# Performance work log

Measured on AMD Instinct MI355X. Metric: run time of the kernel, lower is better.

## Reference

```python
import jax, jax.numpy as jnp
import numpy as np

H, O, E, V = 128, 128, 512, 34
B, T, L = 64, 2048, 256


def _lstm(x, wih, whh, bih, bhh):
    # x: [T, B, Din] -> outputs [T, B, H]; PyTorch gate order i, f, g, o
    n = whh.shape[1]
    h0 = jnp.zeros((x.shape[1], n), x.dtype)
    b = bih + bhh
    def step(carry, xt):
        h, c = carry
        g = xt @ wih.T + h @ whh.T + b
        i, f, gg, o = jnp.split(g, 4, axis=-1)
        c = jax.nn.sigmoid(f) * c + jax.nn.sigmoid(i) * jnp.tanh(gg)
        h = jax.nn.sigmoid(o) * jnp.tanh(c)
        return (h, c), h
    _, ys = jax.lax.scan(step, (h0, h0), x)
    return ys


def _conv1d_s2(x, w, b):
    # x: [B, Cin, T], w: [Cout, Cin, 2], kernel=2 stride=2 valid
    y = jax.lax.conv_general_dilated(x, w, (2,), 'VALID', dimension_numbers=('NCH', 'OIH', 'NCH'))
    return y + b[None, :, None]


def setup_inputs():
    key = jax.random.key(0)
    ctr = [0]
    def mk(shape, s=0.05):
        ctr[0] += 1
        return jax.random.normal(jax.random.fold_in(key, ctr[0]), shape, dtype=jnp.float32) * s
    inp = {}
    inp['utter'] = mk((B, T, 40), 1.0)
    inp['targets'] = jax.random.randint(jax.random.fold_in(key, 999), (B, L), 0, V)
    inp['wih_f'] = mk((4 * H, 40)); inp['whh_f'] = mk((4 * H, H)); inp['bih_f'] = mk((4 * H,)); inp['bhh_f'] = mk((4 * H,))
    inp['wih_r'] = mk((4 * H, 40)); inp['whh_r'] = mk((4 * H, H)); inp['bih_r'] = mk((4 * H,)); inp['bhh_r'] = mk((4 * H,))
    inp['c1w'] = mk((H, 2 * H, 2)); inp['c1b'] = mk((H,))
    inp['wih1'] = mk((4 * H, H)); inp['whh1'] = mk((4 * H, H)); inp['bih1'] = mk((4 * H,)); inp['bhh1'] = mk((4 * H,))
    inp['c2w'] = mk((H, H, 2)); inp['c2b'] = mk((H,))
    inp['wih2'] = mk((4 * H, H)); inp['whh2'] = mk((4 * H, H)); inp['bih2'] = mk((4 * H,)); inp['bhh2'] = mk((4 * H,))
    inp['kw'] = mk((O, H)); inp['kb'] = mk((O,)); inp['vw'] = mk((O, H)); inp['vb'] = mk((O,))
    inp['wihd'] = mk((4 * O, O + E)); inp['whhd'] = mk((4 * O, O)); inp['bihd'] = mk((4 * O,)); inp['bhhd'] = mk((4 * O,))
    inp['w1'] = mk((V, O)); inp['b1'] = mk((V,)); inp['w2'] = mk((V, O)); inp['b2'] = mk((V,))
    inp['w3'] = mk((V, V)); inp['b3'] = mk((V,))
    inp['emb'] = mk((V, E), 1.0)
    inp['sh0'] = mk((B, O)); inp['sc0'] = mk((B, O))
    return inp


def _forward(utter, targets, wih_f, whh_f, bih_f, bhh_f, wih_r, whh_r, bih_r, bhh_r,
             c1w, c1b, wih1, whh1, bih1, bhh1, c2w, c2b, wih2, whh2, bih2, bhh2,
             kw, kb, vw, vb, wihd, whhd, bihd, bhhd, w1, b1, w2, b2, w3, b3,
             emb, sh0, sc0):
    # ---- Listener (encoder) ----
    x = jnp.transpose(utter, (1, 0, 2))            # [T, B, 40]
    fwd = _lstm(x, wih_f, whh_f, bih_f, bhh_f)
    bwd = _lstm(x[::-1], wih_r, whh_r, bih_r, bhh_r)[::-1]
    h = jnp.concatenate([fwd, bwd], axis=-1)       # [T, B, 2H]
    h = jnp.transpose(h, (1, 2, 0))                # [B, 2H, T]
    h = _conv1d_s2(h, c1w, c1b)                    # [B, H, T/2]
    h = jnp.transpose(h, (2, 0, 1))                # [T/2, B, H]
    h = _lstm(h, wih1, whh1, bih1, bhh1)
    h = jnp.transpose(h, (1, 2, 0))
    h = _conv1d_s2(h, c2w, c2b)                    # [B, H, T/4]
    h = jnp.transpose(h, (2, 0, 1))
    h = _lstm(h, wih2, whh2, bih2, bhh2)
    h = jnp.transpose(h, (1, 0, 2))                # [B, T/4, H]
    hk = h @ kw.T + kb                              # [B, T/4, O]
    hv = h @ vw.T + vb
    # ---- Speller (decoder) ----
    ys = jnp.transpose(emb[targets], (1, 0, 2))[:-1]   # [L-1, B, E]
    mask = jnp.ones((utter.shape[0], hk.shape[1]), utter.dtype)  # all full-length
    bd = bihd + bhhd
    def step(carry, y_in):
        c, sh, sc = carry
        g = jnp.concatenate([y_in, c], axis=1) @ wihd.T + sh @ whhd.T + bd
        i, f, gg, o = jnp.split(g, 4, axis=-1)
        sc_n = jax.nn.sigmoid(f) * sc + jax.nn.sigmoid(i) * jnp.tanh(gg)
        sh_n = jax.nn.sigmoid(o) * jnp.tanh(sc_n)
        # NOTE: original attends with the cell state sc (faithful to source)
        att = jax.nn.softmax(jnp.einsum('btd,bd->bt', hk, sc_n), axis=1) * mask
        att = att / jnp.sum(att, axis=1, keepdims=True)
        c_n = jnp.einsum('bt,btd->bd', att, hv)
        out = jax.nn.relu(sh_n @ w1.T + b1 + c_n @ w2.T + b2)
        out = jax.nn.softmax(out @ w3.T + b3, axis=1)
        return (c_n, sh_n, sc_n), out
    c0 = jnp.zeros_like(sh0)
    _, preds = jax.lax.scan(step, (c0, sh0, sc0), ys)
    return jnp.transpose(preds, (1, 0, 2))         # [B, L-1, V]


def reference(utter, targets, wih_f, whh_f, bih_f, bhh_f, wih_r, whh_r, bih_r, bhh_r,
              c1w, c1b, wih1, whh1, bih1, bhh1, c2w, c2b, wih2, whh2, bih2, bhh2,
              kw, kb, vw, vb, wihd, whhd, bihd, bhhd, w1, b1, w2, b2, w3, b3,
              emb, sh0, sc0):
    return _forward(utter, targets, wih_f, whh_f, bih_f, bhh_f, wih_r, whh_r, bih_r, bhh_r,
                    c1w, c1b, wih1, whh1, bih1, bhh1, c2w, c2b, wih2, whh2, bih2, bhh2,
                    kw, kb, vw, vb, wihd, whhd, bihd, bhhd, w1, b1, w2, b2, w3, b3,
                    emb, sh0, sc0)
```

## Files before the change

kernel.cpp:

```cpp
#include <hip/hip_runtime.h>

typedef _Float16 half_t;
typedef _Float16 __attribute__((ext_vector_type(2))) half2_t;

__device__ __forceinline__ float fdot2_(half2_t a, half2_t b, float c) {
#if __has_builtin(__builtin_amdgcn_fdot2)
    return __builtin_amdgcn_fdot2(a, b, c, false);
#else
    return c + (float)a[0] * (float)b[0] + (float)a[1] * (float)b[1];
#endif
}
__device__ __forceinline__ half2_t h2(float a, float b) {
    half2_t r; r[0] = (half_t)a; r[1] = (half_t)b; return r;
}
__device__ __forceinline__ half2_t bc2(unsigned int u) {
    return __builtin_bit_cast(half2_t, u);
}
__device__ __forceinline__ float sigm(float x) { return 1.0f / (1.0f + __expf(-x)); }
__device__ __forceinline__ float tanh_(float x) { return 1.0f - 2.0f / (1.0f + __expf(2.0f * x)); }
__device__ __forceinline__ unsigned int packbf2(float a, float b) {
    unsigned int ua = __float_as_uint(a);
    ua = (ua + 0x7fffu + ((ua >> 16) & 1u)) >> 16;
    unsigned int ub = __float_as_uint(b);
    ub = (ub + 0x7fffu + ((ub >> 16) & 1u)) >> 16;
    return ua | (ub << 16);
}
__device__ __forceinline__ float blo(unsigned int u) { return __uint_as_float(u << 16); }
__device__ __forceinline__ float bhi(unsigned int u) { return __uint_as_float(u & 0xffff0000u); }

__global__ __launch_bounds__(512) void lstm1_k(
    const float* __restrict__ utter,
    const float* __restrict__ wih_f, const float* __restrict__ whh_f,
    const float* __restrict__ bih_f, const float* __restrict__ bhh_f,
    const float* __restrict__ wih_r, const float* __restrict__ whh_r,
    const float* __restrict__ bih_r, const float* __restrict__ bhh_r,
    float* __restrict__ Hf, float* __restrict__ Hr)
{
    const int tid = threadIdx.x;
    const int b   = blockIdx.x & 63;
    const int dir = blockIdx.x >> 6;
    const float* wih = dir ? wih_r : wih_f;
    const float* whh = dir ? whh_r : whh_f;
    const float* bih = dir ? bih_r : bih_f;
    const float* bhh = dir ? bhh_r : bhh_f;
    float* Hout = dir ? Hr : Hf;

    __shared__ float gates[512];
    __shared__ __align__(16) half_t h_h[128];
    __shared__ __align__(16) half_t x2[3][48];

    const int j = tid;
    half2_t wr2[64];
    {
        const float4* wp = reinterpret_cast<const float4*>(whh + j * 128);
#pragma unroll
        for (int m = 0; m < 32; ++m) {
            float4 v = wp[m];
            wr2[2 * m]     = h2(v.x, v.y);
            wr2[2 * m + 1] = h2(v.z, v.w);
        }
    }
    half2_t wx2[20];
    {
        const float4* xp = reinterpret_cast<const float4*>(wih + j * 40);
#pragma unroll
        for (int q = 0; q < 10; ++q) {
            float4 v = xp[q];
            wx2[2 * q]     = h2(v.x, v.y);
            wx2[2 * q + 1] = h2(v.z, v.w);
        }
    }
    const float bias = bih[j] + bhh[j];
    float c = 0.0f;
    if (tid < 128) h_h[tid] = (half_t)0.0f;
    if (tid < 40) {
        int tt0 = dir ? 2047 : 0;
        x2[0][tid] = (half_t)utter[((size_t)b * 2048 + tt0) * 40 + tid];
    } else if (tid < 80) {
        int tt1 = dir ? 2046 : 1;
        x2[1][tid - 40] = (half_t)utter[((size_t)b * 2048 + tt1) * 40 + (tid - 40)];
    }
    __syncthreads();

    for (int t = 0; t < 2048; ++t) {
        const int cur = t % 3;
        const int nx2 = (t + 2) % 3;
        float xn = 0.0f;
        const int tq = tid - 128;
        if (tq >= 0 && tq < 40) {
            int tn = (t + 2 < 2048) ? (t + 2) : 2047;
            int ttn = dir ? (2047 - tn) : tn;
            xn = utter[((size_t)b * 2048 + ttn) * 40 + tq];
        }
        float g0 = bias, g1 = 0.f, g2 = 0.f, g3 = 0.f;
        {
            const uint4* x4p = reinterpret_cast<const uint4*>(&x2[cur][0]);
#pragma unroll
            for (int q = 0; q < 5; ++q) {
                uint4 u = x4p[q];
                g0 = fdot2_(wx2[4 * q],     bc2(u.x), g0);
                g1 = fdot2_(wx2[4 * q + 1], bc2(u.y), g1);
                g2 = fdot2_(wx2[4 * q + 2], bc2(u.z), g2);
                g3 = fdot2_(wx2[4 * q + 3], bc2(u.w), g3);
            }
            const uint4* h4p = reinterpret_cast<const uint4*>(h_h);
#pragma unroll
            for (int q = 0; q < 16; ++q) {
                uint4 u = h4p[q];
                g0 = fdot2_(wr2[4 * q],     bc2(u.x), g0);
                g1 = fdot2_(wr2[4 * q + 1], bc2(u.y), g1);
                g2 = fdot2_(wr2[4 * q + 2], bc2(u.z), g2);
                g3 = fdot2_(wr2[4 * q + 3], bc2(u.w), g3);
            }
        }
        gates[j] = (g0 + g1) + (g2 + g3);
        __syncthreads();
        if (tid < 128) {
            float i_ = sigm(gates[tid]);
            float f_ = sigm(gates[128 + tid]);
            float g_ = tanh_(gates[256 + tid]);
            float o_ = sigm(gates[384 + tid]);
            c = f_ * c + i_ * g_;
            float hh = o_ * tanh_(c);
            h_h[tid] = (half_t)hh;
            int tt = dir ? (2047 - t) : t;
            Hout[((size_t)tt * 64 + b) * 128 + tid] = hh;
        } else if (tq < 40) {
            x2[nx2][tq] = (half_t)xn;
        }
        __syncthreads();
    }
}

__global__ __launch_bounds__(512) void lstm_k(
    const float* __restrict__ P, const float* __restrict__ whh,
    float* __restrict__ Hout, int T)
{
    const int tid = threadIdx.x;
    const int b = blockIdx.x;
    const int j = tid;
    __shared__ float gates[512];
    __shared__ __align__(16) half_t h_h[128];
    half2_t wr2[64];
    {
        const float4* wp = reinterpret_cast<const float4*>(whh + j * 128);
#pragma unroll
        for (int m = 0; m < 32; ++m) {
            float4 v = wp[m];
            wr2[2 * m]     = h2(v.x, v.y);
            wr2[2 * m + 1] = h2(v.z, v.w);
        }
    }
    float c = 0.0f;
    if (tid < 128) h_h[tid] = (half_t)0.0f;
    float p_cur = P[((size_t)b * T + 0) * 512 + j];
    float p_n1  = P[((size_t)b * T + ((T > 1) ? 1 : 0)) * 512 + j];
    __syncthreads();
    for (int t = 0; t < T; ++t) {
        int tn = (t + 2 < T) ? (t + 2) : (T - 1);
        float p_n2 = P[((size_t)b * T + tn) * 512 + j];
        float g0 = p_cur, g1 = 0.f, g2 = 0.f, g3 = 0.f;
        const uint4* h4p = reinterpret_cast<const uint4*>(h_h);
#pragma unroll
        for (int q = 0; q < 16; ++q) {
            uint4 u = h4p[q];
            g0 = fdot2_(wr2[4 * q],     bc2(u.x), g0);
            g1 = fdot2_(wr2[4 * q + 1], bc2(u.y), g1);
            g2 = fdot2_(wr2[4 * q + 2], bc2(u.z), g2);
            g3 = fdot2_(wr2[4 * q + 3], bc2(u.w), g3);
        }
        gates[j] = (g0 + g1) + (g2 + g3);
        __syncthreads();
        if (tid < 128) {
            float i_ = sigm(gates[tid]);
            float f_ = sigm(gates[128 + tid]);
            float g_ = tanh_(gates[256 + tid]);
            float o_ = sigm(gates[384 + tid]);
            c = f_ * c + i_ * g_;
            float hh = o_ * tanh_(c);
            h_h[tid] = (half_t)hh;
            Hout[((size_t)t * 64 + b) * 128 + tid] = hh;
        }
        __syncthreads();
        p_cur = p_n1;
        p_n1 = p_n2;
    }
}

template <int CIN>
__global__ __launch_bounds__(128) void conv_k(
    const float* __restrict__ HA, const float* __restrict__ HB,
    const float* __restrict__ W, const float* __restrict__ bias,
    float* __restrict__ out, int Tout)
{
    __shared__ __align__(16) float xin[64 * CIN];
    const int b = blockIdx.x;
    const int t0 = blockIdx.y * 32;
    const int tid = threadIdx.x;
    for (int idx = tid; idx < 64 * CIN; idx += 128) {
        int tl = idx / CIN, ci = idx % CIN;
        int tau = t0 * 2 + tl;
        float v;
        if constexpr (CIN == 256) {
            v = (ci < 128) ? HA[(size_t)tau * 8192 + b * 128 + ci]
                           : HB[(size_t)tau * 8192 + b * 128 + (ci - 128)];
        } else {
            v = HA[(size_t)tau * 8192 + b * 128 + ci];
        }
        xin[idx] = v;
    }
    __syncthreads();
    const int co = tid;
    float acc[32];
#pragma unroll
    for (int u = 0; u < 32; ++u) acc[u] = 0.0f;
    const float4* Wrow4 = reinterpret_cast<const float4*>(W + (size_t)co * 2 * CIN);
    const float4* xin4 = reinterpret_cast<const float4*>(xin);
    for (int c4 = 0; c4 < CIN / 4; ++c4) {
        float4 wA = Wrow4[2 * c4];
        float4 wB = Wrow4[2 * c4 + 1];
#pragma unroll
        for (int u = 0; u < 32; ++u) {
            float4 x0 = xin4[(2 * u) * (CIN / 4) + c4];
            float4 x1 = xin4[(2 * u + 1) * (CIN / 4) + c4];
            acc[u] += wA.x * x0.x + wA.y * x1.x + wA.z * x0.y + wA.w * x1.y
                    + wB.x * x0.z + wB.y * x1.z + wB.z * x0.w + wB.w * x1.w;
        }
    }
    float bs = bias[co];
#pragma unroll
    for (int u = 0; u < 32; ++u)
        out[((size_t)b * Tout + t0 + u) * 128 + co] = acc[u] + bs;
}

__global__ __launch_bounds__(256) void gemm_k(
    const float* __restrict__ A, const float* __restrict__ W, int ldw,
    const float* __restrict__ bias1, const float* __restrict__ bias2,
    float* __restrict__ C, int M, int N, int K, int mode, int Tdim)
{
    __shared__ __align__(16) float As[16][68];
    __shared__ __align__(16) float Ws[16][68];
    const int tid = threadIdx.x;
    const int m0 = blockIdx.x * 64, n0 = blockIdx.y * 64;
    const int kk = tid & 15, mm = tid >> 4;
    const int tm = tid & 15, tn = tid >> 4;
    float acc[4][4];
#pragma unroll
    for (int i = 0; i < 4; ++i)
#pragma unroll
        for (int jj = 0; jj < 4; ++jj) acc[i][jj] = 0.0f;

    for (int k0 = 0; k0 < K; k0 += 16) {
#pragma unroll
        for (int r = 0; r < 4; ++r) {
            As[kk][mm + 16 * r] = A[(size_t)(m0 + mm + 16 * r) * K + k0 + kk];
            Ws[kk][mm + 16 * r] = W[(size_t)(n0 + mm + 16 * r) * ldw + k0 + kk];
        }
        __syncthreads();
#pragma unroll
        for (int q = 0; q < 16; ++q) {
            float4 a = reinterpret_cast<const float4*>(&As[q][0])[tm];
            float4 w = reinterpret_cast<const float4*>(&Ws[q][0])[tn];
            acc[0][0] += a.x * w.x; acc[0][1] += a.x * w.y; acc[0][2] += a.x * w.z; acc[0][3] += a.x * w.w;
            acc[1][0] += a.y * w.x; acc[1][1] += a.y * w.y; acc[1][2] += a.y * w.z; acc[1][3] += a.y * w.w;
            acc[2][0] += a.z * w.x; acc[2][1] += a.z * w.y; acc[2][2] += a.z * w.z; acc[2][3] += a.z * w.w;
            acc[3][0] += a.w * w.x; acc[3][1] += a.w * w.y; acc[3][2] += a.w * w.z; acc[3][3] += a.w * w.w;
        }
        __syncthreads();
    }
    float bv[4];
#pragma unroll
    for (int jj = 0; jj < 4; ++jj) {
        int n = n0 + tn * 4 + jj;
        float v = 0.0f;
        if (bias1) v += bias1[n];
        if (bias2) v += bias2[n];
        bv[jj] = v;
    }
#pragma unroll
    for (int i = 0; i < 4; ++i) {
        int m = m0 + tm * 4 + i;
#pragma unroll
        for (int jj = 0; jj < 4; ++jj) {
            int n = n0 + tn * 4 + jj;
            float v = acc[i][jj] + bv[jj];
            if (mode == 0) {
                C[(size_t)m * N + n] = v;
            } else {
                int bb = m & 63, tt = m >> 6;
                C[((size_t)bb * N + n) * Tdim + tt] = v;
            }
        }
    }
}

__global__ __launch_bounds__(512) void packemb_k(
    const int* __restrict__ targets, const float* __restrict__ emb,
    float* __restrict__ Ypack)
{
    int m = blockIdx.x;
    int l = m >> 6, b = m & 63;
    int tgt = targets[b * 256 + l];
    Ypack[(size_t)m * 512 + threadIdx.x] = emb[(size_t)tgt * 512 + threadIdx.x];
}

__global__ __launch_bounds__(1024) void decoder_k(
    const float* __restrict__ Yp, const float* __restrict__ whhd, const float* __restrict__ wihd,
    const float* __restrict__ hk,
    const float* __restrict__ hv,
    const float* __restrict__ w1, const float* __restrict__ b1,
    const float* __restrict__ w2, const float* __restrict__ b2,
    const float* __restrict__ w3, const float* __restrict__ b3,
    const float* __restrict__ sh0, const float* __restrict__ sc0,
    float* __restrict__ out)
{
    __shared__ unsigned int hk_lds[512][66];
    __shared__ __align__(16) float partial[32][128];
    __shared__ __align__(16) float sh_f[128];
    __shared__ __align__(16) half_t sh_h[128];
    __shared__ __align__(16) float sc_f[128];
    __shared__ __align__(16) float c_f[128];
    __shared__ __align__(16) half_t c_h[128];
    __shared__ __align__(16) float att[512];
    __shared__ float red[8];
    __shared__ float pa[34], pb[34], z_lds[34];
    __shared__ float w3_lds[34 * 34];
    __shared__ float b3_lds[34];

    const int tid = threadIdx.x;
    const int b = blockIdx.x;
    const int role = tid >> 9;
    const int j = tid & 511;
    float* pflat = &partial[0][0];

    half2_t w2r[64];
    {
        const float4* wp = role
            ? reinterpret_cast<const float4*>(wihd + (size_t)j * 640 + 512)
            : reinterpret_cast<const float4*>(whhd + (size_t)j * 128);
#pragma unroll
        for (int m = 0; m < 32; ++m) {
            float4 v = wp[m];
            w2r[2 * m]     = h2(v.x, v.y);
            w2r[2 * m + 1] = h2(v.z, v.w);
        }
    }
    {
        const float4* hp = reinterpret_cast<const float4*>(hk + ((size_t)j * 64 + b) * 128 + role * 64);
#pragma unroll
        for (int q = 0; q < 16; ++q) {
            float4 v = hp[q];
            hk_lds[j][role * 32 + 2 * q]     = packbf2(v.x, v.y);
            hk_lds[j][role * 32 + 2 * q + 1] = packbf2(v.z, v.w);
        }
    }
    for (int idx = tid; idx < 34 * 34; idx += 1024) w3_lds[idx] = w3[idx];
    if (tid < 34) b3_lds[tid] = b3[tid];
    float sc_r = 0.0f;
    if (tid < 128) {
        float s = sh0[b * 128 + tid];
        sh_f[tid] = s; sh_h[tid] = (half_t)s;
        sc_r = sc0[b * 128 + tid];
        sc_f[tid] = sc_r;
        c_f[tid] = 0.0f; c_h[tid] = (half_t)0.0f;
    }
    __syncthreads();

    const int wid = tid >> 6, lane = tid & 63;
    const int tg = tid >> 5, dq = tid & 31;
    float yp_cur = (role == 0) ? Yp[(size_t)b * 512 + j] : 0.0f;

    for (int l = 0; l < 255; ++l) {
        int lnxt = (l + 1 < 255) ? (l + 1) : l;
        float yp_nxt = (role == 0) ? Yp[((size_t)lnxt * 64 + b) * 512 + j] : 0.0f;
        {
            const uint4* s4 = reinterpret_cast<const uint4*>(role ? c_h : sh_h);
            float g0 = yp_cur, g1 = 0.f, g2 = 0.f, g3 = 0.f;
#pragma unroll
            for (int q = 0; q < 16; ++q) {
                uint4 u = s4[q];
                g0 = fdot2_(w2r[4 * q],     bc2(u.x), g0);
                g1 = fdot2_(w2r[4 * q + 1], bc2(u.y), g1);
                g2 = fdot2_(w2r[4 * q + 2], bc2(u.z), g2);
                g3 = fdot2_(w2r[4 * q + 3], bc2(u.w), g3);
            }
            pflat[tid] = (g0 + g1) + (g2 + g3);
        }
        __syncthreads();
        if (tid < 128) {
            float i_ = sigm(pflat[tid]       + pflat[512 + tid]);
            float f_ = sigm(pflat[128 + tid] + pflat[640 + tid]);
            float g_ = tanh_(pflat[256 + tid] + pflat[768 + tid]);
            float o_ = sigm(pflat[384 + tid] + pflat[896 + tid]);
            sc_r = f_ * sc_r + i_ * g_;
            float hh = o_ * tanh_(sc_r);
            sh_f[tid] = hh; sh_h[tid] = (half_t)hh;
            sc_f[tid] = sc_r;
        }
        __syncthreads();
        if (tid < 512) {
            float e0 = 0.f, e1 = 0.f, e2 = 0.f, e3 = 0.f;
            const uint2* hkr = reinterpret_cast<const uint2*>(&hk_lds[tid][0]);
            const float4* sc4 = reinterpret_cast<const float4*>(sc_f);
#pragma unroll
            for (int q = 0; q < 32; ++q) {
                uint2 u = hkr[q];
                float4 s = sc4[q];
                e0 += blo(u.x) * s.x; e1 += bhi(u.x) * s.y;
                e2 += blo(u.y) * s.z; e3 += bhi(u.y) * s.w;
            }
            float p = __expf((e0 + e1) + (e2 + e3));
            att[tid] = p;
            float ps = p;
#pragma unroll
            for (int off = 32; off; off >>= 1) ps += __shfl_xor(ps, off);
            if (lane == 0) red[wid] = ps;
        }
        __syncthreads();
        {
            const float* hvp = hv + ((size_t)(tg * 16) * 64 + b) * 128 + dq * 4;
            float4 a = make_float4(0.f, 0.f, 0.f, 0.f);
#pragma unroll 4
            for (int tt = 0; tt < 16; ++tt) {
                float w = att[tg * 16 + tt];
                float4 v = *reinterpret_cast<const float4*>(hvp + (size_t)tt * 8192);
                a.x += w * v.x; a.y += w * v.y; a.z += w * v.z; a.w += w * v.w;
            }
            *reinterpret_cast<float4*>(&partial[tg][dq * 4]) = a;
        }
        __syncthreads();
        if (tid < 128) {
            float S = ((red[0] + red[1]) + (red[2] + red[3]))
                    + ((red[4] + red[5]) + (red[6] + red[7]));
            float cs = 0.f;
#pragma unroll
            for (int g = 0; g < 32; ++g) cs += partial[g][tid];
            float cv = cs / S;
            c_f[tid] = cv; c_h[tid] = (half_t)cv;
        }
        __syncthreads();
        if (tid < 34) {
            float o1 = b1[tid];
            const float4* w1r = reinterpret_cast<const float4*>(w1 + tid * 128);
            const float4* sh4 = reinterpret_cast<const float4*>(sh_f);
#pragma unroll 8
            for (int q = 0; q < 32; ++q) {
                float4 a = w1r[q], h = sh4[q];
                o1 += a.x * h.x + a.y * h.y + a.z * h.z + a.w * h.w;
            }
            pa[tid] = o1;
        } else if (tid >= 64 && tid < 98) {
            int v = tid - 64;
            float o2 = b2[v];
            const float4* w2p = reinterpret_cast<const float4*>(w2 + v * 128);
            const float4* c4 = reinterpret_cast<const float4*>(c_f);
#pragma unroll 8
            for (int q = 0; q < 32; ++q) {
                float4 a = w2p[q], cc = c4[q];
                o2 += a.x * cc.x + a.y * cc.y + a.z * cc.z + a.w * cc.w;
            }
            pb[v] = o2;
        }
        __syncthreads();
        if (tid < 34) {
            float z = b3_lds[tid];
            const float* w3r = &w3_lds[tid * 34];
            for (int v = 0; v < 34; ++v) z += w3r[v] * fmaxf(pa[v] + pb[v], 0.0f);
            z_lds[tid] = z;
        }
        __syncthreads();
        if (tid < 34) {
            float zm = z_lds[0];
            for (int v = 1; v < 34; ++v) zm = fmaxf(zm, z_lds[v]);
            float Ssum = 0.0f;
            for (int v = 0; v < 34; ++v) Ssum += __expf(z_lds[v] - zm);
            out[((size_t)b * 255 + l) * 34 + tid] = __expf(z_lds[tid] - zm) / Ssum;
        }
        yp_cur = yp_nxt;
        __syncthreads();
    }
}

extern "C" void kernel_launch(void* const* d_in, const int* in_sizes, int n_in,
                              void* d_out, int out_size, void* d_ws, size_t ws_size,
                              hipStream_t stream) {
    (void)in_sizes; (void)n_in; (void)out_size; (void)ws_size;
    const float* utter = (const float*)d_in[0];
    const int*   targets = (const int*)d_in[1];
    const float* wih_f = (const float*)d_in[2];
    const float* whh_f = (const float*)d_in[3];
    const float* bih_f = (const float*)d_in[4];
    const float* bhh_f = (const float*)d_in[5];
    const float* wih_r = (const float*)d_in[6];
    const float* whh_r = (const float*)d_in[7];
    const float* bih_r = (const float*)d_in[8];
    const float* bhh_r = (const float*)d_in[9];
    const float* c1w = (const float*)d_in[10];
    const float* c1b = (const float*)d_in[11];
    const float* wih1 = (const float*)d_in[12];
    const float* whh1 = (const float*)d_in[13];
    const float* bih1 = (const float*)d_in[14];
    const float* bhh1 = (const float*)d_in[15];
    const float* c2w = (const float*)d_in[16];
    const float* c2b = (const float*)d_in[17];
    const float* wih2 = (const float*)d_in[18];
    const float* whh2 = (const float*)d_in[19];
    const float* bih2 = (const float*)d_in[20];
    const float* bhh2 = (const float*)d_in[21];
    const float* kw = (const float*)d_in[22];
    const float* kb = (const float*)d_in[23];
    const float* vw = (const float*)d_in[24];
    const float* vb = (const float*)d_in[25];
    const float* wihd = (const float*)d_in[26];
    const float* whhd = (const float*)d_in[27];
    const float* bihd = (const float*)d_in[28];
    const float* bhhd = (const float*)d_in[29];
    const float* w1 = (const float*)d_in[30];
    const float* b1 = (const float*)d_in[31];
    const float* w2 = (const float*)d_in[32];
    const float* b2 = (const float*)d_in[33];
    const float* w3 = (const float*)d_in[34];
    const float* b3 = (const float*)d_in[35];
    const float* emb = (const float*)d_in[36];
    const float* sh0 = (const float*)d_in[37];
    const float* sc0 = (const float*)d_in[38];

    char* ws = (char*)d_ws;
    const size_t MB = 1ull << 20;
    float* Hf       = (float*)(ws + 0);
    float* Hr       = (float*)(ws + 64 * MB);
    float* conv1out = (float*)(ws + 128 * MB);
    float* P2       = (float*)(ws + 0);
    float* H2       = (float*)(ws + 128 * MB);
    float* conv2out = (float*)(ws + 0);
    float* P3       = (float*)(ws + 16 * MB);
    float* H3       = (float*)(ws + 80 * MB);
    float* hkb      = (float*)(ws + 96 * MB);
    float* hvb      = (float*)(ws + 112 * MB);
    float* Ypack    = (float*)(ws + 128 * MB);
    float* Yp       = (float*)(ws + 16 * MB);

    lstm1_k<<<128, 512, 0, stream>>>(utter, wih_f, whh_f, bih_f, bhh_f,
                                     wih_r, whh_r, bih_r, bhh_r, Hf, Hr);
    conv_k<256><<<dim3(64, 32), 128, 0, stream>>>(Hf, Hr, c1w, c1b, conv1out, 1024);
    gemm_k<<<dim3(1024, 8), 256, 0, stream>>>(conv1out, wih1, 128, bih1, bhh1,
                                              P2, 65536, 512, 128, 0, 0);
    lstm_k<<<64, 512, 0, stream>>>(P2, whh1, H2, 1024);
    conv_k<128><<<dim3(64, 16), 128, 0, stream>>>(H2, nullptr, c2w, c2b, conv2out, 512);
    gemm_k<<<dim3(512, 8), 256, 0, stream>>>(conv2out, wih2, 128, bih2, bhh2,
                                             P3, 32768, 512, 128, 0, 0);
    lstm_k<<<64, 512, 0, stream>>>(P3, whh2, H3, 512);
    gemm_k<<<dim3(512, 2), 256, 0, stream>>>(H3, kw, 128, kb, nullptr,
                                             hkb, 32768, 128, 128, 0, 0);
    gemm_k<<<dim3(512, 2), 256, 0, stream>>>(H3, vw, 128, vb, nullptr,
                                             hvb, 32768, 128, 128, 0, 0);
    packemb_k<<<16320, 512, 0, stream>>>(targets, emb, Ypack);
    gemm_k<<<dim3(255, 8), 256, 0, stream>>>(Ypack, wihd, 640, bihd, bhhd,
                                             Yp, 16320, 512, 512, 0, 0);
    decoder_k<<<64, 1024, 0, stream>>>(Yp, whhd, wihd, hkb, hvb,
                                       w1, b1, w2, b2, w3, b3, sh0, sc0,
                                       (float*)d_out);
}
```

Measured before the change: 5.999 ms.

## Restructure decoder to 512 threads with bf16-packed transposed values and pinned weights

The decoder now runs 512 threads per block, and each thread holds both the recurrent and context input weight rows, so the gate partial-sum reduction goes away. The attention value tensor is written transposed by the GEMM and packed to bf16 by a new kernel, so the context reduction reads contiguous packed rows instead of strided fp32 global loads. Weights are kept as packed uints pinned with empty asm, with launch bounds (512,1) in the LSTM kernels, to keep them in registers. The trailing barrier in the decoder loop is removed. The costs are an extra launch, bf16 rounding of the values, and higher register pressure.

```diff
diff --git a/kernel.cpp b/kernel.cpp
--- a/kernel.cpp
+++ b/kernel.cpp
@@ -15,6 +15,9 @@
 }
 __device__ __forceinline__ half2_t bc2(unsigned int u) {
     return __builtin_bit_cast(half2_t, u);
+}
+__device__ __forceinline__ unsigned int pk2(float a, float b) {
+    return __builtin_bit_cast(unsigned int, h2(a, b));
 }
 __device__ __forceinline__ float sigm(float x) { return 1.0f / (1.0f + __expf(-x)); }
 __device__ __forceinline__ float tanh_(float x) { return 1.0f - 2.0f / (1.0f + __expf(2.0f * x)); }
@@ -28,7 +31,9 @@
 __device__ __forceinline__ float blo(unsigned int u) { return __uint_as_float(u << 16); }
 __device__ __forceinline__ float bhi(unsigned int u) { return __uint_as_float(u & 0xffff0000u); }
 
-__global__ __launch_bounds__(512) void lstm1_k(
+#define PIN(v) asm volatile("" : "+v"(v))
+
+__global__ __launch_bounds__(512, 1) void lstm1_k(
     const float* __restrict__ utter,
     const float* __restrict__ wih_f, const float* __restrict__ whh_f,
     const float* __restrict__ bih_f, const float* __restrict__ bhh_f,
@@ -50,26 +55,30 @@
     __shared__ __align__(16) half_t x2[3][48];
 
     const int j = tid;
-    half2_t wr2[64];
+    unsigned int wr2[64];
     {
         const float4* wp = reinterpret_cast<const float4*>(whh + j * 128);
 #pragma unroll
         for (int m = 0; m < 32; ++m) {
             float4 v = wp[m];
-            wr2[2 * m]     = h2(v.x, v.y);
-            wr2[2 * m + 1] = h2(v.z, v.w);
-        }
-    }
-    half2_t wx2[20];
+            wr2[2 * m]     = pk2(v.x, v.y);
+            wr2[2 * m + 1] = pk2(v.z, v.w);
+        }
+    }
+#pragma unroll
+    for (int m = 0; m < 64; ++m) PIN(wr2[m]);
+    unsigned int wx2[20];
     {
         const float4* xp = reinterpret_cast<const float4*>(wih + j * 40);
 #pragma unroll
         for (int q = 0; q < 10; ++q) {
             float4 v = xp[q];
-            wx2[2 * q]     = h2(v.x, v.y);
-            wx2[2 * q + 1] = h2(v.z, v.w);
-        }
-    }
+            wx2[2 * q]     = pk2(v.x, v.y);
+            wx2[2 * q + 1] = pk2(v.z, v.w);
+        }
+    }
+#pragma unroll
+    for (int q = 0; q < 20; ++q) PIN(wx2[q]);
     const float bias = bih[j] + bhh[j];
     float c = 0.0f;
     if (tid < 128) h_h[tid] = (half_t)0.0f;
@@ -98,19 +107,19 @@
 #pragma unroll
             for (int q = 0; q < 5; ++q) {
                 uint4 u = x4p[q];
-                g0 = fdot2_(wx2[4 * q],     bc2(u.x), g0);
-                g1 = fdot2_(wx2[4 * q + 1], bc2(u.y), g1);
-                g2 = fdot2_(wx2[4 * q + 2], bc2(u.z), g2);
-                g3 = fdot2_(wx2[4 * q + 3], bc2(u.w), g3);
+                g0 = fdot2_(bc2(wx2[4 * q]),     bc2(u.x), g0);
+                g1 = fdot2_(bc2(wx2[4 * q + 1]), bc2(u.y), g1);
+                g2 = fdot2_(bc2(wx2[4 * q + 2]), bc2(u.z), g2);
+                g3 = fdot2_(bc2(wx2[4 * q + 3]), bc2(u.w), g3);
             }
             const uint4* h4p = reinterpret_cast<const uint4*>(h_h);
 #pragma unroll
             for (int q = 0; q < 16; ++q) {
                 uint4 u = h4p[q];
-                g0 = fdot2_(wr2[4 * q],     bc2(u.x), g0);
-                g1 = fdot2_(wr2[4 * q + 1], bc2(u.y), g1);
-                g2 = fdot2_(wr2[4 * q + 2], bc2(u.z), g2);
-                g3 = fdot2_(wr2[4 * q + 3], bc2(u.w), g3);
+                g0 = fdot2_(bc2(wr2[4 * q]),     bc2(u.x), g0);
+                g1 = fdot2_(bc2(wr2[4 * q + 1]), bc2(u.y), g1);
+                g2 = fdot2_(bc2(wr2[4 * q + 2]), bc2(u.z), g2);
+                g3 = fdot2_(bc2(wr2[4 * q + 3]), bc2(u.w), g3);
             }
         }
         gates[j] = (g0 + g1) + (g2 + g3);
@@ -132,7 +141,7 @@
     }
 }
 
-__global__ __launch_bounds__(512) void lstm_k(
+__global__ __launch_bounds__(512, 1) void lstm_k(
     const float* __restrict__ P, const float* __restrict__ whh,
     float* __restrict__ Hout, int T)
 {
@@ -141,16 +150,18 @@
     const int j = tid;
     __shared__ float gates[512];
     __shared__ __align__(16) half_t h_h[128];
-    half2_t wr2[64];
+    unsigned int wr2[64];
     {
         const float4* wp = reinterpret_cast<const float4*>(whh + j * 128);
 #pragma unroll
         for (int m = 0; m < 32; ++m) {
             float4 v = wp[m];
-            wr2[2 * m]     = h2(v.x, v.y);
-            wr2[2 * m + 1] = h2(v.z, v.w);
-        }
-    }
+            wr2[2 * m]     = pk2(v.x, v.y);
+            wr2[2 * m + 1] = pk2(v.z, v.w);
+        }
+    }
+#pragma unroll
+    for (int m = 0; m < 64; ++m) PIN(wr2[m]);
     float c = 0.0f;
     if (tid < 128) h_h[tid] = (half_t)0.0f;
     float p_cur = P[((size_t)b * T + 0) * 512 + j];
@@ -164,10 +175,10 @@
 #pragma unroll
         for (int q = 0; q < 16; ++q) {
             uint4 u = h4p[q];
-            g0 = fdot2_(wr2[4 * q],     bc2(u.x), g0);
-            g1 = fdot2_(wr2[4 * q + 1], bc2(u.y), g1);
-            g2 = fdot2_(wr2[4 * q + 2], bc2(u.z), g2);
-            g3 = fdot2_(wr2[4 * q + 3], bc2(u.w), g3);
+            g0 = fdot2_(bc2(wr2[4 * q]),     bc2(u.x), g0);
+            g1 = fdot2_(bc2(wr2[4 * q + 1]), bc2(u.y), g1);
+            g2 = fdot2_(bc2(wr2[4 * q + 2]), bc2(u.z), g2);
+            g3 = fdot2_(bc2(wr2[4 * q + 3]), bc2(u.w), g3);
         }
         gates[j] = (g0 + g1) + (g2 + g3);
         __syncthreads();
@@ -304,10 +315,18 @@
     Ypack[(size_t)m * 512 + threadIdx.x] = emb[(size_t)tgt * 512 + threadIdx.x];
 }
 
-__global__ __launch_bounds__(1024) void decoder_k(
+__global__ __launch_bounds__(256) void packhv_k(
+    const float* __restrict__ hvT, unsigned int* __restrict__ hvpak)
+{
+    int b = blockIdx.x, d = blockIdx.y, i = threadIdx.x;
+    const float2 v = reinterpret_cast<const float2*>(hvT + ((size_t)b * 128 + d) * 512)[i];
+    hvpak[((size_t)b * 128 + d) * 256 + i] = packbf2(v.x, v.y);
+}
+
+__global__ __launch_bounds__(512, 1) void decoder_k(
     const float* __restrict__ Yp, const float* __restrict__ whhd, const float* __restrict__ wihd,
     const float* __restrict__ hk,
-    const float* __restrict__ hv,
+    const unsigned int* __restrict__ hvpak,
     const float* __restrict__ w1, const float* __restrict__ b1,
     const float* __restrict__ w2, const float* __restrict__ b2,
     const float* __restrict__ w3, const float* __restrict__ b3,
@@ -315,7 +334,7 @@
     float* __restrict__ out)
 {
     __shared__ unsigned int hk_lds[512][66];
-    __shared__ __align__(16) float partial[32][128];
+    __shared__ float gates[512];
     __shared__ __align__(16) float sh_f[128];
     __shared__ __align__(16) half_t sh_h[128];
     __shared__ __align__(16) float sc_f[128];
@@ -329,32 +348,33 @@
 
     const int tid = threadIdx.x;
     const int b = blockIdx.x;
-    const int role = tid >> 9;
-    const int j = tid & 511;
-    float* pflat = &partial[0][0];
-
-    half2_t w2r[64];
+
+    unsigned int whp[64], wcp[64];
     {
-        const float4* wp = role
-            ? reinterpret_cast<const float4*>(wihd + (size_t)j * 640 + 512)
-            : reinterpret_cast<const float4*>(whhd + (size_t)j * 128);
+        const float4* wp = reinterpret_cast<const float4*>(whhd + (size_t)tid * 128);
+        const float4* cp = reinterpret_cast<const float4*>(wihd + (size_t)tid * 640 + 512);
 #pragma unroll
         for (int m = 0; m < 32; ++m) {
             float4 v = wp[m];
-            w2r[2 * m]     = h2(v.x, v.y);
-            w2r[2 * m + 1] = h2(v.z, v.w);
-        }
-    }
+            whp[2 * m]     = pk2(v.x, v.y);
+            whp[2 * m + 1] = pk2(v.z, v.w);
+            float4 w = cp[m];
+            wcp[2 * m]     = pk2(w.x, w.y);
+            wcp[2 * m + 1] = pk2(w.z, w.w);
+        }
+    }
+#pragma unroll
+    for (int m = 0; m < 64; ++m) { PIN(whp[m]); PIN(wcp[m]); }
     {
-        const float4* hp = reinterpret_cast<const float4*>(hk + ((size_t)j * 64 + b) * 128 + role * 64);
-#pragma unroll
-        for (int q = 0; q < 16; ++q) {
+        const float4* hp = reinterpret_cast<const float4*>(hk + ((size_t)tid * 64 + b) * 128);
+#pragma unroll
+        for (int q = 0; q < 32; ++q) {
             float4 v = hp[q];
-            hk_lds[j][role * 32 + 2 * q]     = packbf2(v.x, v.y);
-            hk_lds[j][role * 32 + 2 * q + 1] = packbf2(v.z, v.w);
-        }
-    }
-    for (int idx = tid; idx < 34 * 34; idx += 1024) w3_lds[idx] = w3[idx];
+            hk_lds[tid][2 * q]     = packbf2(v.x, v.y);
+            hk_lds[tid][2 * q + 1] = packbf2(v.z, v.w);
+        }
+    }
+    for (int idx = tid; idx < 34 * 34; idx += 512) w3_lds[idx] = w3[idx];
     if (tid < 34) b3_lds[tid] = b3[tid];
     float sc_r = 0.0f;
     if (tid < 128) {
@@ -367,38 +387,48 @@
     __syncthreads();
 
     const int wid = tid >> 6, lane = tid & 63;
-    const int tg = tid >> 5, dq = tid & 31;
-    float yp_cur = (role == 0) ? Yp[(size_t)b * 512 + j] : 0.0f;
+    const int g4 = tid >> 7, d = tid & 127;
+    const uint4* hvr = reinterpret_cast<const uint4*>(hvpak + ((size_t)b * 128 + d) * 256 + g4 * 64);
+    float yp_cur = Yp[(size_t)b * 512 + tid];
 
     for (int l = 0; l < 255; ++l) {
         int lnxt = (l + 1 < 255) ? (l + 1) : l;
-        float yp_nxt = (role == 0) ? Yp[((size_t)lnxt * 64 + b) * 512 + j] : 0.0f;
+        float yp_nxt = Yp[((size_t)lnxt * 64 + b) * 512 + tid];
         {
-            const uint4* s4 = reinterpret_cast<const uint4*>(role ? c_h : sh_h);
             float g0 = yp_cur, g1 = 0.f, g2 = 0.f, g3 = 0.f;
+            const uint4* s4 = reinterpret_cast<const uint4*>(sh_h);
 #pragma unroll
             for (int q = 0; q < 16; ++q) {
                 uint4 u = s4[q];
-                g0 = fdot2_(w2r[4 * q],     bc2(u.x), g0);
-                g1 = fdot2_(w2r[4 * q + 1], bc2(u.y), g1);
-                g2 = fdot2_(w2r[4 * q + 2], bc2(u.z), g2);
-                g3 = fdot2_(w2r[4 * q + 3], bc2(u.w), g3);
-            }
-            pflat[tid] = (g0 + g1) + (g2 + g3);
+                g0 = fdot2_(bc2(whp[4 * q]),     bc2(u.x), g0);
+                g1 = fdot2_(bc2(whp[4 * q + 1]), bc2(u.y), g1);
+                g2 = fdot2_(bc2(whp[4 * q + 2]), bc2(u.z), g2);
+                g3 = fdot2_(bc2(whp[4 * q + 3]), bc2(u.w), g3);
+            }
+            const uint4* c4p = reinterpret_cast<const uint4*>(c_h);
+#pragma unroll
+            for (int q = 0; q < 16; ++q) {
+                uint4 u = c4p[q];
+                g0 = fdot2_(bc2(wcp[4 * q]),     bc2(u.x), g0);
+                g1 = fdot2_(bc2(wcp[4 * q + 1]), bc2(u.y), g1);
+                g2 = fdot2_(bc2(wcp[4 * q + 2]), bc2(u.z), g2);
+                g3 = fdot2_(bc2(wcp[4 * q + 3]), bc2(u.w), g3);
+            }
+            gates[tid] = (g0 + g1) + (g2 + g3);
         }
         __syncthreads();
         if (tid < 128) {
-            float i_ = sigm(pflat[tid]       + pflat[512 + tid]);
-            float f_ = sigm(pflat[128 + tid] + pflat[640 + tid]);
-            float g_ = tanh_(pflat[256 + tid] + pflat[768 + tid]);
-            float o_ = sigm(pflat[384 + tid] + pflat[896 + tid]);
+            float i_ = sigm(gates[tid]);
+            float f_ = sigm(gates[128 + tid]);
+            float g_ = tanh_(gates[256 + tid]);
+            float o_ = sigm(gates[384 + tid]);
             sc_r = f_ * sc_r + i_ * g_;
             float hh = o_ * tanh_(sc_r);
             sh_f[tid] = hh; sh_h[tid] = (half_t)hh;
             sc_f[tid] = sc_r;
         }
         __syncthreads();
-        if (tid < 512) {
+        {
             float e0 = 0.f, e1 = 0.f, e2 = 0.f, e3 = 0.f;
             const uint2* hkr = reinterpret_cast<const uint2*>(&hk_lds[tid][0]);
             const float4* sc4 = reinterpret_cast<const float4*>(sc_f);
@@ -418,24 +448,23 @@
         }
         __syncthreads();
         {
-            const float* hvp = hv + ((size_t)(tg * 16) * 64 + b) * 128 + dq * 4;
-            float4 a = make_float4(0.f, 0.f, 0.f, 0.f);
-#pragma unroll 4
-            for (int tt = 0; tt < 16; ++tt) {
-                float w = att[tg * 16 + tt];
-                float4 v = *reinterpret_cast<const float4*>(hvp + (size_t)tt * 8192);
-                a.x += w * v.x; a.y += w * v.y; a.z += w * v.z; a.w += w * v.w;
-            }
-            *reinterpret_cast<float4*>(&partial[tg][dq * 4]) = a;
+            const float4* att4 = reinterpret_cast<const float4*>(att);
+            float acc = 0.0f;
+#pragma unroll
+            for (int q = 0; q < 16; ++q) {
+                uint4 u = hvr[q];
+                float4 a0 = att4[g4 * 32 + 2 * q];
+                float4 a1 = att4[g4 * 32 + 2 * q + 1];
+                acc += blo(u.x) * a0.x + bhi(u.x) * a0.y + blo(u.y) * a0.z + bhi(u.y) * a0.w
+                     + blo(u.z) * a1.x + bhi(u.z) * a1.y + blo(u.w) * a1.z + bhi(u.w) * a1.w;
+            }
+            gates[tid] = acc;
         }
         __syncthreads();
         if (tid < 128) {
             float S = ((red[0] + red[1]) + (red[2] + red[3]))
                     + ((red[4] + red[5]) + (red[6] + red[7]));
-            float cs = 0.f;
-#pragma unroll
-            for (int g = 0; g < 32; ++g) cs += partial[g][tid];
-            float cv = cs / S;
+            float cv = (gates[tid] + gates[128 + tid] + gates[256 + tid] + gates[384 + tid]) / S;
             c_f[tid] = cv; c_h[tid] = (half_t)cv;
         }
         __syncthreads();
@@ -477,7 +506,6 @@
             out[((size_t)b * 255 + l) * 34 + tid] = __expf(z_lds[tid] - zm) / Ssum;
         }
         yp_cur = yp_nxt;
-        __syncthreads();
     }
 }
 
@@ -536,7 +564,8 @@
     float* P3       = (float*)(ws + 16 * MB);
     float* H3       = (float*)(ws + 80 * MB);
     float* hkb      = (float*)(ws + 96 * MB);
-    float* hvb      = (float*)(ws + 112 * MB);
+    float* hvT      = (float*)(ws + 112 * MB);
+    unsigned int* hvpak = (unsigned int*)(ws + 0);
     float* Ypack    = (float*)(ws + 128 * MB);
     float* Yp       = (float*)(ws + 16 * MB);
 
@@ -553,11 +582,12 @@
     gemm_k<<<dim3(512, 2), 256, 0, stream>>>(H3, kw, 128, kb, nullptr,
                                              hkb, 32768, 128, 128, 0, 0);
     gemm_k<<<dim3(512, 2), 256, 0, stream>>>(H3, vw, 128, vb, nullptr,
-                                             hvb, 32768, 128, 128, 0, 0);
+                                             hvT, 32768, 128, 128, 1, 512);
+    packhv_k<<<dim3(64, 128), 256, 0, stream>>>(hvT, hvpak);
     packemb_k<<<16320, 512, 0, stream>>>(targets, emb, Ypack);
     gemm_k<<<dim3(255, 8), 256, 0, stream>>>(Ypack, wihd, 640, bihd, bhhd,
                                              Yp, 16320, 512, 512, 0, 0);
-    decoder_k<<<64, 1024, 0, stream>>>(Yp, whhd, wihd, hkb, hvb,
-                                       w1, b1, w2, b2, w3, b3, sh0, sc0,
-                                       (float*)d_out);
-}
+    decoder_k<<<64, 512, 0, stream>>>(Yp, whhd, wihd, hkb, hvpak,
+                                      w1, b1, w2, b2, w3, b3, sh0, sc0,
+                                      (float*)d_out);
+}
```

Result: slower. 7.044 ms (+17.4%).
